# Kernel tuning notes

Measured on AMD Instinct MI355X. Metric: run time of the kernel, lower is better.

The kernel has to match this reference:

```python
import jax, jax.numpy as jnp
import numpy as np

FFT_N = 320.0  # one-sided 161-bin spectrum of a 320-point FFT


def setup_inputs() -> dict:
    key = jax.random.key(0)
    spec = jax.random.normal(key, (32, 4000, 161, 2), dtype=jnp.float32)
    return {"spec": spec}


def _frame_gain(spec):
    # spec: [B, T, F, 2] -> per-frame RMS gain g0: [B, T]
    spec_pow = jnp.sum(spec * spec, axis=-1)  # [B, T, F]
    p = (jnp.sum(spec_pow[..., 1:-1], axis=-1) * 2.0
         + spec_pow[..., 0] + spec_pow[..., -1]) / FFT_N  # [B, T]
    return jnp.sqrt(p)


def _ema_over_time(g0):
    # g[0] = g0[0]; g[n] = 0.9*g[n-1] + 0.1*g0[n]  (scan over time axis 1)
    def step(carry, x):
        c = carry * 0.9 + x * 0.1
        return c, c
    init = g0[:, 0]                       # [B]
    xs = jnp.swapaxes(g0[:, 1:], 0, 1)    # [T-1, B]
    _, outs = jax.lax.scan(step, init, xs)  # [T-1, B]
    return jnp.concatenate([g0[:, :1], jnp.swapaxes(outs, 0, 1)], axis=1)  # [B, T]


def reference(spec):
    g0 = _frame_gain(spec)                        # [B, T]
    gain = _ema_over_time(g0)[:, :, None, None]   # [B, T, 1, 1]
    new_spec = spec / (gain + 0.001)              # [B, T, F, 2]
    return new_spec, gain
```

## Files before the change

kernel.cpp:

```cpp
#include <hip/hip_runtime.h>


typedef float f32x4 __attribute__((ext_vector_type(4)));
typedef float f32x2 __attribute__((ext_vector_type(2)));

#define B_SZ 32
#define T_SZ 4000
#define FRAME_F 322
#define FRAMES (B_SZ * T_SZ)
#define N_SPEC ((size_t)FRAMES * FRAME_F)
#define N4 (N_SPEC / 4)
#define EMA_W 384
#define BLOCK 256

__global__ __launch_bounds__(BLOCK) void k_frame_gain(
    const float* __restrict__ spec, float* __restrict__ g0) {
  int lane   = threadIdx.x & 63;
  int wave0  = (blockIdx.x * BLOCK + threadIdx.x) >> 6;
  int nwaves = (gridDim.x * BLOCK) >> 6;
#pragma unroll 2
  for (int wid = wave0; wid < FRAMES; wid += nwaves) {
    const float* fp = spec + (size_t)wid * FRAME_F;
    f32x4 v0 = *(const f32x4*)(fp + lane * 4);
    float s0 = v0.x * v0.x + v0.y * v0.y;
    float s1 = v0.z * v0.z + v0.w * v0.w;
    float acc = 2.0f * (s0 + s1);
    if (lane == 0) acc -= s0;
    if (lane < 16) {
      f32x4 v1 = *(const f32x4*)(fp + (64 + lane) * 4);
      acc += 2.0f * (v1.x * v1.x + v1.y * v1.y + v1.z * v1.z + v1.w * v1.w);
    } else if (lane == 16) {
      f32x2 v2 = *(const f32x2*)(fp + 320);
      acc += v2.x * v2.x + v2.y * v2.y;
    }
#pragma unroll
    for (int off = 32; off > 0; off >>= 1) acc += __shfl_xor(acc, off, 64);
    if (lane == 0) g0[wid] = sqrtf(acc * (1.0f / 320.0f));
  }
}

__global__ __launch_bounds__(BLOCK) void k_ema(
    const float* __restrict__ g0, float* __restrict__ gain_out,
    float* __restrict__ inv_out) {
  __shared__ float xs[EMA_W + 256];
  int b  = blockIdx.y;
  int t0 = blockIdx.x * 256;
  int lo = t0 - (EMA_W - 1); if (lo < 0) lo = 0;
  int hi = t0 + 256; if (hi > T_SZ) hi = T_SZ;
  int n  = hi - lo;
  const float* gb = g0 + b * T_SZ;

  for (int i = threadIdx.x; i < n; i += BLOCK) xs[i] = gb[lo + i];
  __syncthreads();

  int t = t0 + (int)threadIdx.x;
  if (t >= T_SZ) return;
  int s = t - (EMA_W - 1); if (s < 1) s = 1;
  float c = (s == 1) ? xs[0] : 0.f;
  for (int k = s; k <= t; ++k) c = c * 0.9f + xs[k - lo] * 0.1f;
  gain_out[b * T_SZ + t] = c;
  inv_out[b * T_SZ + t]  = 1.0f / (c + 0.001f);
}

__global__ __launch_bounds__(BLOCK) void k_apply(
    const float* __restrict__ spec, const float* __restrict__ inv_g,
    float* __restrict__ out) {
  size_t stride = (size_t)gridDim.x * BLOCK;
#pragma unroll 2
  for (size_t i = (size_t)blockIdx.x * BLOCK + threadIdx.x; i < N4; i += stride) {
    f32x4 v = ((const f32x4*)spec)[i];
    unsigned p0 = (unsigned)(2 * i);
    unsigned f0 = p0 / 161u;
    unsigned f1 = (p0 + 1) / 161u;
    float inv0 = inv_g[f0];
    float inv1 = inv_g[f1];
    f32x4 r;
    r.x = v.x * inv0; r.y = v.y * inv0;
    r.z = v.z * inv1; r.w = v.w * inv1;
    __builtin_nontemporal_store(r, (f32x4*)out + i);
  }
}

extern "C" void kernel_launch(void* const* d_in, const int* in_sizes, int n_in,
                              void* d_out, int out_size, void* d_ws, size_t ws_size,
                              hipStream_t stream) {
  const float* spec = (const float*)d_in[0];
  float* out   = (float*)d_out;
  float* gain  = out + N_SPEC;
  float* g0    = (float*)d_ws;
  float* inv_g = g0 + FRAMES;

  k_frame_gain<<<1024, BLOCK, 0, stream>>>(spec, g0);

  dim3 g2((T_SZ + 255) / 256, B_SZ);
  k_ema<<<g2, BLOCK, 0, stream>>>(g0, gain, inv_g);

  k_apply<<<2048, BLOCK, 0, stream>>>(spec, inv_g, out);
}
```

Baseline: 114.0 us.

## Replace grid-stride loops with one-shot blocks and stage inverse gains in LDS

The frame-gain kernel now launches one wave per frame instead of a persistent grid-stride loop. The apply kernel gives each block a fixed contiguous chunk of 16 vec4s per thread. It preloads that chunk's inverse gains into shared memory and computes the second frame index from the division remainder, which saves one integer division per element. The output store changes from nontemporal to a regular store, which may pollute the cache. The many small blocks add launch and scheduling overhead in exchange for more parallelism and less per-element global indexing.

```diff
diff --git a/kernel.cpp b/kernel.cpp
--- a/kernel.cpp
+++ b/kernel.cpp
@@ -11,41 +11,43 @@
 #define N_SPEC ((size_t)FRAMES * FRAME_F)
 #define N4 (N_SPEC / 4)
 #define EMA_W 384
+#define HALO (EMA_W - 1)
 #define BLOCK 256
+#define U 16
+#define APB (BLOCK * U)
 
 __global__ __launch_bounds__(BLOCK) void k_frame_gain(
     const float* __restrict__ spec, float* __restrict__ g0) {
-  int lane   = threadIdx.x & 63;
-  int wave0  = (blockIdx.x * BLOCK + threadIdx.x) >> 6;
-  int nwaves = (gridDim.x * BLOCK) >> 6;
-#pragma unroll 2
-  for (int wid = wave0; wid < FRAMES; wid += nwaves) {
-    const float* fp = spec + (size_t)wid * FRAME_F;
-    f32x4 v0 = *(const f32x4*)(fp + lane * 4);
-    float s0 = v0.x * v0.x + v0.y * v0.y;
-    float s1 = v0.z * v0.z + v0.w * v0.w;
-    float acc = 2.0f * (s0 + s1);
-    if (lane == 0) acc -= s0;
-    if (lane < 16) {
-      f32x4 v1 = *(const f32x4*)(fp + (64 + lane) * 4);
-      acc += 2.0f * (v1.x * v1.x + v1.y * v1.y + v1.z * v1.z + v1.w * v1.w);
-    } else if (lane == 16) {
-      f32x2 v2 = *(const f32x2*)(fp + 320);
-      acc += v2.x * v2.x + v2.y * v2.y;
-    }
+  int gtid = blockIdx.x * BLOCK + threadIdx.x;
+  int wid  = gtid >> 6;
+  int lane = threadIdx.x & 63;
+  if (wid >= FRAMES) return;
+
+  const float* fp = spec + (size_t)wid * FRAME_F;
+  f32x4 v0 = *(const f32x4*)(fp + lane * 4);
+  float s0 = v0.x * v0.x + v0.y * v0.y;
+  float s1 = v0.z * v0.z + v0.w * v0.w;
+  float acc = 2.0f * (s0 + s1);
+  if (lane == 0) acc -= s0;
+  if (lane < 16) {
+    f32x4 v1 = *(const f32x4*)(fp + (64 + lane) * 4);
+    acc += 2.0f * (v1.x * v1.x + v1.y * v1.y + v1.z * v1.z + v1.w * v1.w);
+  } else if (lane == 16) {
+    f32x2 v2 = *(const f32x2*)(fp + 320);
+    acc += v2.x * v2.x + v2.y * v2.y;
+  }
 #pragma unroll
-    for (int off = 32; off > 0; off >>= 1) acc += __shfl_xor(acc, off, 64);
-    if (lane == 0) g0[wid] = sqrtf(acc * (1.0f / 320.0f));
-  }
+  for (int off = 32; off > 0; off >>= 1) acc += __shfl_xor(acc, off, 64);
+  if (lane == 0) g0[wid] = sqrtf(acc * (1.0f / 320.0f));
 }
 
 __global__ __launch_bounds__(BLOCK) void k_ema(
     const float* __restrict__ g0, float* __restrict__ gain_out,
     float* __restrict__ inv_out) {
-  __shared__ float xs[EMA_W + 256];
+  __shared__ float xs[HALO + 1 + 256];
   int b  = blockIdx.y;
   int t0 = blockIdx.x * 256;
-  int lo = t0 - (EMA_W - 1); if (lo < 0) lo = 0;
+  int lo = t0 - HALO; if (lo < 0) lo = 0;
   int hi = t0 + 256; if (hi > T_SZ) hi = T_SZ;
   int n  = hi - lo;
   const float* gb = g0 + b * T_SZ;
@@ -55,7 +57,7 @@
 
   int t = t0 + (int)threadIdx.x;
   if (t >= T_SZ) return;
-  int s = t - (EMA_W - 1); if (s < 1) s = 1;
+  int s = t - HALO; if (s < 1) s = 1;
   float c = (s == 1) ? xs[0] : 0.f;
   for (int k = s; k <= t; ++k) c = c * 0.9f + xs[k - lo] * 0.1f;
   gain_out[b * T_SZ + t] = c;
@@ -65,19 +67,31 @@
 __global__ __launch_bounds__(BLOCK) void k_apply(
     const float* __restrict__ spec, const float* __restrict__ inv_g,
     float* __restrict__ out) {
-  size_t stride = (size_t)gridDim.x * BLOCK;
-#pragma unroll 2
-  for (size_t i = (size_t)blockIdx.x * BLOCK + threadIdx.x; i < N4; i += stride) {
-    f32x4 v = ((const f32x4*)spec)[i];
-    unsigned p0 = (unsigned)(2 * i);
-    unsigned f0 = p0 / 161u;
-    unsigned f1 = (p0 + 1) / 161u;
-    float inv0 = inv_g[f0];
-    float inv1 = inv_g[f1];
-    f32x4 r;
-    r.x = v.x * inv0; r.y = v.y * inv0;
-    r.z = v.z * inv1; r.w = v.w * inv1;
-    __builtin_nontemporal_store(r, (f32x4*)out + i);
+  __shared__ float linv[56];
+  size_t b0 = (size_t)blockIdx.x * APB;
+  unsigned fA = (unsigned)(2 * b0) / 161u;
+  size_t lastI = b0 + APB - 1; if (lastI > N4 - 1) lastI = N4 - 1;
+  unsigned fB = (unsigned)(2 * lastI + 1) / 161u;
+  if (threadIdx.x < fB - fA + 1) linv[threadIdx.x] = inv_g[fA + threadIdx.x];
+  __syncthreads();
+
+#pragma unroll
+  for (int k = 0; k < U; ++k) {
+    size_t i = b0 + threadIdx.x + (size_t)k * BLOCK;
+    if (i < N4) {
+      f32x4 v = ((const f32x4*)spec)[i];
+      unsigned p = (unsigned)(2 * i);
+      unsigned q = p / 161u;
+      unsigned r = p - q * 161u;
+      unsigned l0 = q - fA;
+      unsigned l1 = l0 + (r == 160u);
+      float i0 = linv[l0];
+      float i1 = linv[l1];
+      f32x4 rr;
+      rr.x = v.x * i0; rr.y = v.y * i0;
+      rr.z = v.z * i1; rr.w = v.w * i1;
+      ((f32x4*)out)[i] = rr;
+    }
   }
 }
 
@@ -90,10 +104,11 @@
   float* g0    = (float*)d_ws;
   float* inv_g = g0 + FRAMES;
 
-  k_frame_gain<<<1024, BLOCK, 0, stream>>>(spec, g0);
+  k_frame_gain<<<(FRAMES + 3) / 4, BLOCK, 0, stream>>>(spec, g0);
 
   dim3 g2((T_SZ + 255) / 256, B_SZ);
   k_ema<<<g2, BLOCK, 0, stream>>>(g0, gain, inv_g);
 
-  k_apply<<<2048, BLOCK, 0, stream>>>(spec, inv_g, out);
+  int blocks3 = (int)((N4 + APB - 1) / APB);
+  k_apply<<<blocks3, BLOCK, 0, stream>>>(spec, inv_g, out);
 }
```

New measurement: 109.4 us. 4.0% less time.

## Use thread-per-frame gain reduction and one-element-per-thread apply kernel

Applied to the files above, without the earlier changes.

The frame-gain kernel now gives each thread a whole frame, with a serial 80-iteration vector loop, instead of a wave-wide shuffle reduction. This removes the cross-lane reduction but makes adjacent lanes read addresses 1288 bytes apart, so loads are poorly coalesced. The apply kernel drops its grid-stride loop and launches one thread per float4. It also replaces the second integer division with a remainder check. The EMA kernel only gets a renamed HALO constant.

```diff
diff --git a/kernel.cpp b/kernel.cpp
--- a/kernel.cpp
+++ b/kernel.cpp
@@ -11,41 +11,38 @@
 #define N_SPEC ((size_t)FRAMES * FRAME_F)
 #define N4 (N_SPEC / 4)
 #define EMA_W 384
+#define HALO (EMA_W - 1)
 #define BLOCK 256
 
 __global__ __launch_bounds__(BLOCK) void k_frame_gain(
     const float* __restrict__ spec, float* __restrict__ g0) {
-  int lane   = threadIdx.x & 63;
-  int wave0  = (blockIdx.x * BLOCK + threadIdx.x) >> 6;
-  int nwaves = (gridDim.x * BLOCK) >> 6;
-#pragma unroll 2
-  for (int wid = wave0; wid < FRAMES; wid += nwaves) {
-    const float* fp = spec + (size_t)wid * FRAME_F;
-    f32x4 v0 = *(const f32x4*)(fp + lane * 4);
-    float s0 = v0.x * v0.x + v0.y * v0.y;
-    float s1 = v0.z * v0.z + v0.w * v0.w;
-    float acc = 2.0f * (s0 + s1);
-    if (lane == 0) acc -= s0;
-    if (lane < 16) {
-      f32x4 v1 = *(const f32x4*)(fp + (64 + lane) * 4);
-      acc += 2.0f * (v1.x * v1.x + v1.y * v1.y + v1.z * v1.z + v1.w * v1.w);
-    } else if (lane == 16) {
-      f32x2 v2 = *(const f32x2*)(fp + 320);
-      acc += v2.x * v2.x + v2.y * v2.y;
-    }
-#pragma unroll
-    for (int off = 32; off > 0; off >>= 1) acc += __shfl_xor(acc, off, 64);
-    if (lane == 0) g0[wid] = sqrtf(acc * (1.0f / 320.0f));
+  int wid = blockIdx.x * BLOCK + threadIdx.x;
+  if (wid >= FRAMES) return;
+  const float* fp = spec + (size_t)wid * FRAME_F;
+
+  float ax = 0.f, ay = 0.f, az = 0.f, aw = 0.f;
+#pragma unroll 10
+  for (int j = 0; j < 80; ++j) {
+    f32x4 v = *(const f32x4*)(fp + j * 4);
+    ax += v.x * v.x; ay += v.y * v.y;
+    az += v.z * v.z; aw += v.w * v.w;
   }
+  f32x2 v0 = *(const f32x2*)(fp);
+  f32x2 vL = *(const f32x2*)(fp + 320);
+  float total = (ax + az) + (ay + aw);
+  float pow0  = v0.x * v0.x + v0.y * v0.y;
+  float powL  = vL.x * vL.x + vL.y * vL.y;
+  float wnum  = 2.f * total - pow0 + powL;
+  g0[wid] = sqrtf(wnum * (1.0f / 320.0f));
 }
 
 __global__ __launch_bounds__(BLOCK) void k_ema(
     const float* __restrict__ g0, float* __restrict__ gain_out,
     float* __restrict__ inv_out) {
-  __shared__ float xs[EMA_W + 256];
+  __shared__ float xs[HALO + 1 + 256];
   int b  = blockIdx.y;
   int t0 = blockIdx.x * 256;
-  int lo = t0 - (EMA_W - 1); if (lo < 0) lo = 0;
+  int lo = t0 - HALO; if (lo < 0) lo = 0;
   int hi = t0 + 256; if (hi > T_SZ) hi = T_SZ;
   int n  = hi - lo;
   const float* gb = g0 + b * T_SZ;
@@ -55,7 +52,7 @@
 
   int t = t0 + (int)threadIdx.x;
   if (t >= T_SZ) return;
-  int s = t - (EMA_W - 1); if (s < 1) s = 1;
+  int s = t - HALO; if (s < 1) s = 1;
   float c = (s == 1) ? xs[0] : 0.f;
   for (int k = s; k <= t; ++k) c = c * 0.9f + xs[k - lo] * 0.1f;
   gain_out[b * T_SZ + t] = c;
@@ -65,20 +62,19 @@
 __global__ __launch_bounds__(BLOCK) void k_apply(
     const float* __restrict__ spec, const float* __restrict__ inv_g,
     float* __restrict__ out) {
-  size_t stride = (size_t)gridDim.x * BLOCK;
-#pragma unroll 2
-  for (size_t i = (size_t)blockIdx.x * BLOCK + threadIdx.x; i < N4; i += stride) {
-    f32x4 v = ((const f32x4*)spec)[i];
-    unsigned p0 = (unsigned)(2 * i);
-    unsigned f0 = p0 / 161u;
-    unsigned f1 = (p0 + 1) / 161u;
-    float inv0 = inv_g[f0];
-    float inv1 = inv_g[f1];
-    f32x4 r;
-    r.x = v.x * inv0; r.y = v.y * inv0;
-    r.z = v.z * inv1; r.w = v.w * inv1;
-    __builtin_nontemporal_store(r, (f32x4*)out + i);
-  }
+  size_t i = (size_t)blockIdx.x * BLOCK + threadIdx.x;
+  if (i >= N4) return;
+  f32x4 v = ((const f32x4*)spec)[i];
+  unsigned p0 = (unsigned)(2 * i);
+  unsigned f0 = p0 / 161u;
+  unsigned r  = p0 - f0 * 161u;
+  unsigned f1 = f0 + (r == 160u);
+  float i0 = inv_g[f0];
+  float i1 = inv_g[f1];
+  f32x4 rr;
+  rr.x = v.x * i0; rr.y = v.y * i0;
+  rr.z = v.z * i1; rr.w = v.w * i1;
+  __builtin_nontemporal_store(rr, (f32x4*)out + i);
 }
 
 extern "C" void kernel_launch(void* const* d_in, const int* in_sizes, int n_in,
@@ -90,10 +86,10 @@
   float* g0    = (float*)d_ws;
   float* inv_g = g0 + FRAMES;
 
-  k_frame_gain<<<1024, BLOCK, 0, stream>>>(spec, g0);
+  k_frame_gain<<<(FRAMES + BLOCK - 1) / BLOCK, BLOCK, 0, stream>>>(spec, g0);
 
   dim3 g2((T_SZ + 255) / 256, B_SZ);
   k_ema<<<g2, BLOCK, 0, stream>>>(g0, gain, inv_g);
 
-  k_apply<<<2048, BLOCK, 0, stream>>>(spec, inv_g, out);
+  k_apply<<<(int)((N4 + BLOCK - 1) / BLOCK), BLOCK, 0, stream>>>(spec, inv_g, out);
 }
```

Result: faster. 97.28 us (-14.6%).
